# Kernel optimization log

Measured on AMD Instinct MI355X. Metric: run time of the kernel, lower is better.

## Reference

```python
import jax, jax.numpy as jnp
import numpy as np

NUM_SAMPLES = 1024  # from init_kwargs


def _fps(x, num_samples):
    """Iterative farthest-point sampling.

    x: [B, N, C] float point cloud.
    Returns (sampled_points [B, S, C], indices [B, S] int32).
    Starts from point 0 in each cloud (deterministic seed point).
    """
    B, N, C = x.shape
    barange = jnp.arange(B)
    init_idx = jnp.zeros((B,), dtype=jnp.int32)
    init_min = jnp.full((B, N), jnp.inf, dtype=x.dtype)

    def step(carry, _):
        min_d, cur = carry
        pt = x[barange, cur]                                  # [B, C] current farthest point
        d = jnp.sum((x - pt[:, None, :]) ** 2, axis=-1)       # [B, N] squared dist to it
        min_d = jnp.minimum(min_d, d)                         # running min-dist to sampled set
        nxt = jnp.argmax(min_d, axis=1).astype(jnp.int32)     # next farthest point per cloud
        return (min_d, nxt), cur                              # emit the index we just consumed

    (_, _), idxs = jax.lax.scan(step, (init_min, init_idx), None, length=num_samples)
    idxs = jnp.transpose(idxs)                                # [B, S]
    sampled = jnp.take_along_axis(x, idxs[..., None], axis=1)  # [B, S, C]
    return sampled, idxs


def setup_inputs() -> dict:
    key = jax.random.key(0)
    x = jax.random.uniform(key, (64, 32768, 3), dtype=jnp.float32)
    return {"x": x}


def reference(x):
    return _fps(x, NUM_SAMPLES)
```

## Files before the change

kernel.cpp:

```cpp
#include <hip/hip_runtime.h>


typedef unsigned long long u64;
typedef unsigned int u32;
typedef unsigned short u16;

#define FPS_N   32768
#define FPS_S   1024
#define FPS_NT  1024
#define NCELL   512
#define PPT     (FPS_N / FPS_NT)

__device__ __forceinline__ int bin_of(float v) {
    int i = (int)(v * 8.0f);
    i = i < 0 ? 0 : (i > 7 ? 7 : i);
    if (v < (float)i * 0.125f) --i;
    if (v >= (float)(i + 1) * 0.125f) ++i;
    i = i < 0 ? 0 : (i > 7 ? 7 : i);
    return i;
}

__global__ __launch_bounds__(FPS_NT) void FPSModel_80753975099708_kernel(
    const float* __restrict__ x,
    float* __restrict__ out_pts,
    float* __restrict__ out_idx,
    float4* __restrict__ ws4)
{
#pragma clang fp contract(off)
    const int b = blockIdx.x;
    const int t = threadIdx.x;
    const int w = t >> 6;
    const int lane = t & 63;
    const float* __restrict__ xb = x + (size_t)b * FPS_N * 3;
    float* __restrict__ op = out_pts + (size_t)b * FPS_S * 3;
    float* __restrict__ oi = out_idx + (size_t)b * FPS_S;
    float4* __restrict__ srt = ws4 + (size_t)b * FPS_N;

    __shared__ float mind[FPS_N];
    __shared__ u32  cellCnt[NCELL];
    __shared__ u32  cellStart[NCELL + 1];
    __shared__ u64  bkey[NCELL];
    __shared__ float bwx[NCELL], bwy[NCELL], bwz[NCELL];
    __shared__ u16  wl[2][NCELL];
    __shared__ u32  nD[2];
    __shared__ u64  redk[16];
    __shared__ float redx[16], redy[16], redz[16];

    if (t < NCELL) cellCnt[t] = 0;
    if (t == 0) { nD[0] = 0; nD[1] = 0; }
    __syncthreads();

#pragma unroll
    for (int k = 0; k < PPT; ++k) {
        const int i = k * FPS_NT + t;
        mind[i] = __int_as_float(0x7f800000);
        const float gx = xb[3 * i], gy = xb[3 * i + 1], gz = xb[3 * i + 2];
        const int c = (bin_of(gx) << 6) | (bin_of(gy) << 3) | bin_of(gz);
        atomicAdd(&cellCnt[c], 1u);
    }
    __syncthreads();

    if (t == 0) {
        u32 acc = 0;
        for (int c = 0; c < NCELL; ++c) { cellStart[c] = acc; acc += cellCnt[c]; }
        cellStart[NCELL] = acc;
    }
    __syncthreads();
    if (t < NCELL) cellCnt[t] = cellStart[t];
    __syncthreads();

#pragma unroll
    for (int k = 0; k < PPT; ++k) {
        const int i = k * FPS_NT + t;
        const float gx = xb[3 * i], gy = xb[3 * i + 1], gz = xb[3 * i + 2];
        const int c = (bin_of(gx) << 6) | (bin_of(gy) << 3) | bin_of(gz);
        const u32 slot = atomicAdd(&cellCnt[c], 1u);
        float4 q;
        q.x = gx; q.y = gy; q.z = gz; q.w = __uint_as_float((u32)i);
        srt[slot] = q;
    }
    if (t < NCELL) {
        bkey[t] = (cellStart[t + 1] > cellStart[t])
                      ? 0x7f80000000000000ULL
                      : 0ULL;
        bwx[t] = 0.f; bwy[t] = 0.f; bwz[t] = 0.f;
    }

    float px = xb[0], py = xb[1], pz = xb[2];
    if (t == 0) {
        oi[0] = 0.0f;
        op[0] = px; op[1] = py; op[2] = pz;
    }
    __syncthreads();

    for (int s = 1; s < FPS_S; ++s) {
        const int p = s & 1;
        if (t == 0) nD[1 - p] = 0;
        if (t < NCELL) {
            const int ix = (t >> 6) & 7, iy = (t >> 3) & 7, iz = t & 7;
            const float lox = (float)ix * 0.125f;
            const float loy = (float)iy * 0.125f;
            const float loz = (float)iz * 0.125f;
            const float ax = fmaxf(fmaxf(lox - px, px - (lox + 0.125f)), 0.0f);
            const float ay = fmaxf(fmaxf(loy - py, py - (loy + 0.125f)), 0.0f);
            const float az = fmaxf(fmaxf(loz - pz, pz - (loz + 0.125f)), 0.0f);
            const float lb2 = ax * ax + ay * ay + az * az;
            const float bmax = __uint_as_float((u32)(bkey[t] >> 32));
            if (!(lb2 >= bmax * 1.000004f)) {
                wl[p][atomicAdd(&nD[p], 1u)] = (u16)t;
            }
        }
        __syncthreads();

        const int nd = (int)nD[p];
        for (int wi = w; wi < nd; wi += 16) {
            const int c = wl[p][wi];
            const int start = (int)cellStart[c], end = (int)cellStart[c + 1];
            u64 bk = 0; float bx = 0.f, by = 0.f, bz = 0.f;
            for (int off = start; off < end; off += 64) {
                const int l = off + lane;
                if (l < end) {
                    const float4 q = srt[l];
                    const float dx = q.x - px;
                    const float dy = q.y - py;
                    const float dz = q.z - pz;
                    const float d = __builtin_fmaf(dz, dz,
                                     __builtin_fmaf(dx, dx, dy * dy));
                    const float m = fminf(mind[l], d);
                    mind[l] = m;
                    const u64 key = ((u64)__float_as_uint(m) << 32) |
                                    (u64)(0xFFFFFFFFu - __float_as_uint(q.w));
                    if (key > bk) { bk = key; bx = q.x; by = q.y; bz = q.z; }
                }
            }
#pragma unroll
            for (int o = 32; o; o >>= 1) {
                const u64 ok = __shfl_xor((unsigned long long)bk, o);
                const float ox = __shfl_xor(bx, o);
                const float oy = __shfl_xor(by, o);
                const float oz = __shfl_xor(bz, o);
                if (ok > bk) { bk = ok; bx = ox; by = oy; bz = oz; }
            }
            if (lane == 0) { bkey[c] = bk; bwx[c] = bx; bwy[c] = by; bwz[c] = bz; }
        }
        __syncthreads();

        u64 k = 0; float wx = 0.f, wy = 0.f, wz = 0.f;
        if (t < NCELL) { k = bkey[t]; wx = bwx[t]; wy = bwy[t]; wz = bwz[t]; }
#pragma unroll
        for (int o = 32; o; o >>= 1) {
            const u64 ok = __shfl_xor((unsigned long long)k, o);
            const float ox = __shfl_xor(wx, o);
            const float oy = __shfl_xor(wy, o);
            const float oz = __shfl_xor(wz, o);
            if (ok > k) { k = ok; wx = ox; wy = oy; wz = oz; }
        }
        if (lane == 0) { redk[w] = k; redx[w] = wx; redy[w] = wy; redz[w] = wz; }
        __syncthreads();

        u64 fk = redk[0];
        float fx = redx[0], fy = redy[0], fz = redz[0];
#pragma unroll
        for (int j = 1; j < 16; ++j) {
            const u64 kk = redk[j];
            if (kk > fk) { fk = kk; fx = redx[j]; fy = redy[j]; fz = redz[j]; }
        }
        px = fx; py = fy; pz = fz;

        if (t == 0) {
            oi[s] = (float)(int)(0xFFFFFFFFu - (u32)(fk & 0xFFFFFFFFull));
            op[(size_t)s * 3 + 0] = fx;
            op[(size_t)s * 3 + 1] = fy;
            op[(size_t)s * 3 + 2] = fz;
        }
    }
}

extern "C" void kernel_launch(void* const* d_in, const int* in_sizes, int n_in,
                              void* d_out, int out_size, void* d_ws, size_t ws_size,
                              hipStream_t stream) {
    const float* x = (const float*)d_in[0];
    const int B = in_sizes[0] / (FPS_N * 3);

    float* out_pts = (float*)d_out;
    float* out_idx = out_pts + (size_t)B * FPS_S * 3;
    float4* ws4 = (float4*)d_ws;

    hipLaunchKernelGGL(FPSModel_80753975099708_kernel,
                       dim3(B), dim3(FPS_NT), 0, stream,
                       x, out_pts, out_idx, ws4);
}
```

Measured before the change: 4.493 ms.

## Coarsen grid to 64 cells, compute dirty set per wave via ballot, drop a barrier

Reduces the spatial grid from 512 to 64 cells so every wave can compute the dirty-cell bitmask itself with a ballot over its lanes. This removes the shared worklist, its atomics and one barrier per step. Cell bests are double-buffered, and the final argmax is a serial scan of 64 keys per thread. Coordinates of the new point are reloaded from global memory, and a software prefetch is added to the cell scan loop. The cost is that coarser cells prune less, so more points are rescanned each step, and the dirty cells are load-balanced round-robin across waves.

```diff
diff --git a/kernel.cpp b/kernel.cpp
--- a/kernel.cpp
+++ b/kernel.cpp
@@ -3,20 +3,19 @@
 
 typedef unsigned long long u64;
 typedef unsigned int u32;
-typedef unsigned short u16;
 
 #define FPS_N   32768
 #define FPS_S   1024
 #define FPS_NT  1024
-#define NCELL   512
+#define NCELL   64
 #define PPT     (FPS_N / FPS_NT)
 
-__device__ __forceinline__ int bin_of(float v) {
-    int i = (int)(v * 8.0f);
-    i = i < 0 ? 0 : (i > 7 ? 7 : i);
-    if (v < (float)i * 0.125f) --i;
-    if (v >= (float)(i + 1) * 0.125f) ++i;
-    i = i < 0 ? 0 : (i > 7 ? 7 : i);
+__device__ __forceinline__ int bin4(float v) {
+    int i = (int)(v * 4.0f);
+    i = i < 0 ? 0 : (i > 3 ? 3 : i);
+    if (v < (float)i * 0.25f) --i;
+    if (v >= (float)(i + 1) * 0.25f) ++i;
+    i = i < 0 ? 0 : (i > 3 ? 3 : i);
     return i;
 }
 
@@ -37,17 +36,11 @@
     float4* __restrict__ srt = ws4 + (size_t)b * FPS_N;
 
     __shared__ float mind[FPS_N];
-    __shared__ u32  cellCnt[NCELL];
+    __shared__ u64  bkey[2][NCELL];
     __shared__ u32  cellStart[NCELL + 1];
-    __shared__ u64  bkey[NCELL];
-    __shared__ float bwx[NCELL], bwy[NCELL], bwz[NCELL];
-    __shared__ u16  wl[2][NCELL];
-    __shared__ u32  nD[2];
-    __shared__ u64  redk[16];
-    __shared__ float redx[16], redy[16], redz[16];
+    __shared__ u32  cellCur[NCELL];
 
-    if (t < NCELL) cellCnt[t] = 0;
-    if (t == 0) { nD[0] = 0; nD[1] = 0; }
+    if (t < NCELL) cellCur[t] = 0;
     __syncthreads();
 
 #pragma unroll
@@ -55,35 +48,34 @@
         const int i = k * FPS_NT + t;
         mind[i] = __int_as_float(0x7f800000);
         const float gx = xb[3 * i], gy = xb[3 * i + 1], gz = xb[3 * i + 2];
-        const int c = (bin_of(gx) << 6) | (bin_of(gy) << 3) | bin_of(gz);
-        atomicAdd(&cellCnt[c], 1u);
+        const int c = (bin4(gx) << 4) | (bin4(gy) << 2) | bin4(gz);
+        atomicAdd(&cellCur[c], 1u);
     }
     __syncthreads();
 
     if (t == 0) {
         u32 acc = 0;
-        for (int c = 0; c < NCELL; ++c) { cellStart[c] = acc; acc += cellCnt[c]; }
+        for (int c = 0; c < NCELL; ++c) { cellStart[c] = acc; acc += cellCur[c]; }
         cellStart[NCELL] = acc;
     }
     __syncthreads();
-    if (t < NCELL) cellCnt[t] = cellStart[t];
+    if (t < NCELL) cellCur[t] = cellStart[t];
     __syncthreads();
 
 #pragma unroll
     for (int k = 0; k < PPT; ++k) {
         const int i = k * FPS_NT + t;
         const float gx = xb[3 * i], gy = xb[3 * i + 1], gz = xb[3 * i + 2];
-        const int c = (bin_of(gx) << 6) | (bin_of(gy) << 3) | bin_of(gz);
-        const u32 slot = atomicAdd(&cellCnt[c], 1u);
+        const int c = (bin4(gx) << 4) | (bin4(gy) << 2) | bin4(gz);
+        const u32 slot = atomicAdd(&cellCur[c], 1u);
         float4 q;
         q.x = gx; q.y = gy; q.z = gz; q.w = __uint_as_float((u32)i);
         srt[slot] = q;
     }
     if (t < NCELL) {
-        bkey[t] = (cellStart[t + 1] > cellStart[t])
-                      ? 0x7f80000000000000ULL
-                      : 0ULL;
-        bwx[t] = 0.f; bwy[t] = 0.f; bwz[t] = 0.f;
+        bkey[0][t] = (cellStart[t + 1] > cellStart[t])
+                         ? 0x7f80000000000000ULL
+                         : 0ULL;
     }
 
     float px = xb[0], py = xb[1], pz = xb[2];
@@ -94,84 +86,81 @@
     __syncthreads();
 
     for (int s = 1; s < FPS_S; ++s) {
-        const int p = s & 1;
-        if (t == 0) nD[1 - p] = 0;
-        if (t < NCELL) {
-            const int ix = (t >> 6) & 7, iy = (t >> 3) & 7, iz = t & 7;
-            const float lox = (float)ix * 0.125f;
-            const float loy = (float)iy * 0.125f;
-            const float loz = (float)iz * 0.125f;
-            const float ax = fmaxf(fmaxf(lox - px, px - (lox + 0.125f)), 0.0f);
-            const float ay = fmaxf(fmaxf(loy - py, py - (loy + 0.125f)), 0.0f);
-            const float az = fmaxf(fmaxf(loz - pz, pz - (loz + 0.125f)), 0.0f);
-            const float lb2 = ax * ax + ay * ay + az * az;
-            const float bmax = __uint_as_float((u32)(bkey[t] >> 32));
-            if (!(lb2 >= bmax * 1.000004f)) {
-                wl[p][atomicAdd(&nD[p], 1u)] = (u16)t;
+        const int p  = s & 1;
+        const int qb = p ^ 1;
+
+        const int ix = (lane >> 4) & 3, iy = (lane >> 2) & 3, iz = lane & 3;
+        const float lox = (float)ix * 0.25f;
+        const float loy = (float)iy * 0.25f;
+        const float loz = (float)iz * 0.25f;
+        const float ax = fmaxf(fmaxf(lox - px, px - (lox + 0.25f)), 0.0f);
+        const float ay = fmaxf(fmaxf(loy - py, py - (loy + 0.25f)), 0.0f);
+        const float az = fmaxf(fmaxf(loz - pz, pz - (loz + 0.25f)), 0.0f);
+        const float lb2 = ax * ax + ay * ay + az * az;
+        const u64 prevk = bkey[qb][lane];
+        const float bmax = __uint_as_float((u32)(prevk >> 32));
+        const bool dirty = !(lb2 >= bmax * 1.000004f);
+        const u64 mask = __ballot(dirty);
+
+        if (w == 0 && !dirty) bkey[p][lane] = prevk;
+
+        u64 mrem = mask;
+        int j = 0;
+        while (mrem) {
+            const int c = __ffsll((unsigned long long)mrem) - 1;
+            mrem &= mrem - 1;
+            if ((j & 15) == w) {
+                const int end = (int)cellStart[c + 1];
+                int off = (int)cellStart[c] + lane;
+                u64 bk = 0;
+                float4 q0;
+                if (off < end) q0 = srt[off];
+                while (off < end) {
+                    const int off2 = off + 64;
+                    float4 q1;
+                    if (off2 < end) q1 = srt[off2];
+                    const float dx = q0.x - px;
+                    const float dy = q0.y - py;
+                    const float dz = q0.z - pz;
+                    const float d = __builtin_fmaf(dz, dz,
+                                     __builtin_fmaf(dx, dx, dy * dy));
+                    const float m = fminf(mind[off], d);
+                    mind[off] = m;
+                    const u64 key = ((u64)__float_as_uint(m) << 32) |
+                                    (u64)(0xFFFFFFFFu - __float_as_uint(q0.w));
+                    if (key > bk) bk = key;
+                    q0 = q1;
+                    off = off2;
+                }
+#pragma unroll
+                for (int o = 32; o; o >>= 1) {
+                    const u64 ok = __shfl_xor((unsigned long long)bk, o);
+                    if (ok > bk) bk = ok;
+                }
+                if (lane == 0) bkey[p][c] = bk;
             }
+            ++j;
         }
         __syncthreads();
 
-        const int nd = (int)nD[p];
-        for (int wi = w; wi < nd; wi += 16) {
-            const int c = wl[p][wi];
-            const int start = (int)cellStart[c], end = (int)cellStart[c + 1];
-            u64 bk = 0; float bx = 0.f, by = 0.f, bz = 0.f;
-            for (int off = start; off < end; off += 64) {
-                const int l = off + lane;
-                if (l < end) {
-                    const float4 q = srt[l];
-                    const float dx = q.x - px;
-                    const float dy = q.y - py;
-                    const float dz = q.z - pz;
-                    const float d = __builtin_fmaf(dz, dz,
-                                     __builtin_fmaf(dx, dx, dy * dy));
-                    const float m = fminf(mind[l], d);
-                    mind[l] = m;
-                    const u64 key = ((u64)__float_as_uint(m) << 32) |
-                                    (u64)(0xFFFFFFFFu - __float_as_uint(q.w));
-                    if (key > bk) { bk = key; bx = q.x; by = q.y; bz = q.z; }
-                }
-            }
+        u64 fk = bkey[p][0];
 #pragma unroll
-            for (int o = 32; o; o >>= 1) {
-                const u64 ok = __shfl_xor((unsigned long long)bk, o);
-                const float ox = __shfl_xor(bx, o);
-                const float oy = __shfl_xor(by, o);
-                const float oz = __shfl_xor(bz, o);
-                if (ok > bk) { bk = ok; bx = ox; by = oy; bz = oz; }
-            }
-            if (lane == 0) { bkey[c] = bk; bwx[c] = bx; bwy[c] = by; bwz[c] = bz; }
+        for (int jj = 1; jj < NCELL; ++jj) {
+            const u64 kk = bkey[p][jj];
+            if (kk > fk) fk = kk;
         }
-        __syncthreads();
+        const int cur = (int)(0xFFFFFFFFu - (u32)(fk & 0xFFFFFFFFull));
 
-        u64 k = 0; float wx = 0.f, wy = 0.f, wz = 0.f;
-        if (t < NCELL) { k = bkey[t]; wx = bwx[t]; wy = bwy[t]; wz = bwz[t]; }
-#pragma unroll
-        for (int o = 32; o; o >>= 1) {
-            const u64 ok = __shfl_xor((unsigned long long)k, o);
-            const float ox = __shfl_xor(wx, o);
-            const float oy = __shfl_xor(wy, o);
-            const float oz = __shfl_xor(wz, o);
-            if (ok > k) { k = ok; wx = ox; wy = oy; wz = oz; }
-        }
-        if (lane == 0) { redk[w] = k; redx[w] = wx; redy[w] = wy; redz[w] = wz; }
-        __syncthreads();
-
-        u64 fk = redk[0];
-        float fx = redx[0], fy = redy[0], fz = redz[0];
-#pragma unroll
-        for (int j = 1; j < 16; ++j) {
-            const u64 kk = redk[j];
-            if (kk > fk) { fk = kk; fx = redx[j]; fy = redy[j]; fz = redz[j]; }
-        }
-        px = fx; py = fy; pz = fz;
+        const int curU = __builtin_amdgcn_readfirstlane(cur);
+        px = xb[3 * curU + 0];
+        py = xb[3 * curU + 1];
+        pz = xb[3 * curU + 2];
 
         if (t == 0) {
-            oi[s] = (float)(int)(0xFFFFFFFFu - (u32)(fk & 0xFFFFFFFFull));
-            op[(size_t)s * 3 + 0] = fx;
-            op[(size_t)s * 3 + 1] = fy;
-            op[(size_t)s * 3 + 2] = fz;
+            oi[s] = (float)cur;
+            op[(size_t)s * 3 + 0] = px;
+            op[(size_t)s * 3 + 1] = py;
+            op[(size_t)s * 3 + 2] = pz;
         }
     }
 }
```

Result: faster. 3.800 ms (-15.4%).

## Use fixed 64-point spatially sorted chunks with AABB pruning and ballot worklists

Applied to the files above, without the earlier changes.

Points are still counting-sorted into 512 grid cells, but pruning now works on 512 fixed chunks of 64 consecutive sorted points, each with its own bounding box computed by wave reductions. The dirty-chunk list is built from ballots instead of a shared atomic worklist. Chunk work is split round-robin across waves, with the next chunk loaded before the previous one is processed. The per-chunk winner reduction shuffles only the key and resolves coordinates through a chunk index, cutting shuffle traffic. The tighter boxes should prune more tightly than the fixed grid cells, but chunks can straddle cells and so have looser bounds.

```diff
diff --git a/kernel.cpp b/kernel.cpp
--- a/kernel.cpp
+++ b/kernel.cpp
@@ -3,15 +3,15 @@
 
 typedef unsigned long long u64;
 typedef unsigned int u32;
-typedef unsigned short u16;
 
 #define FPS_N   32768
 #define FPS_S   1024
 #define FPS_NT  1024
-#define NCELL   512
+#define NCH     512
+#define NCELL9  512
 #define PPT     (FPS_N / FPS_NT)
 
-__device__ __forceinline__ int bin_of(float v) {
+__device__ __forceinline__ int bin8(float v) {
     int i = (int)(v * 8.0f);
     i = i < 0 ? 0 : (i > 7 ? 7 : i);
     if (v < (float)i * 0.125f) --i;
@@ -37,17 +37,17 @@
     float4* __restrict__ srt = ws4 + (size_t)b * FPS_N;
 
     __shared__ float mind[FPS_N];
-    __shared__ u32  cellCnt[NCELL];
-    __shared__ u32  cellStart[NCELL + 1];
-    __shared__ u64  bkey[NCELL];
-    __shared__ float bwx[NCELL], bwy[NCELL], bwz[NCELL];
-    __shared__ u16  wl[2][NCELL];
-    __shared__ u32  nD[2];
-    __shared__ u64  redk[16];
-    __shared__ float redx[16], redy[16], redz[16];
-
-    if (t < NCELL) cellCnt[t] = 0;
-    if (t == 0) { nD[0] = 0; nD[1] = 0; }
+    __shared__ float alox[NCH], aloy[NCH], aloz[NCH];
+    __shared__ float ahix[NCH], ahiy[NCH], ahiz[NCH];
+    __shared__ u64  ckey[NCH];
+    __shared__ float cwx[NCH], cwy[NCH], cwz[NCH];
+    __shared__ u64  dmask[8];
+    __shared__ u64  wkey[8];
+    __shared__ u32  wchunk[8];
+    __shared__ u32  cellStart[NCELL9 + 1];
+    __shared__ u32  cellCur[NCELL9];
+
+    if (t < NCELL9) cellCur[t] = 0;
     __syncthreads();
 
 #pragma unroll
@@ -55,35 +55,48 @@
         const int i = k * FPS_NT + t;
         mind[i] = __int_as_float(0x7f800000);
         const float gx = xb[3 * i], gy = xb[3 * i + 1], gz = xb[3 * i + 2];
-        const int c = (bin_of(gx) << 6) | (bin_of(gy) << 3) | bin_of(gz);
-        atomicAdd(&cellCnt[c], 1u);
-    }
-    __syncthreads();
-
+        const int c = (bin8(gx) << 6) | (bin8(gy) << 3) | bin8(gz);
+        atomicAdd(&cellCur[c], 1u);
+    }
+    __syncthreads();
     if (t == 0) {
         u32 acc = 0;
-        for (int c = 0; c < NCELL; ++c) { cellStart[c] = acc; acc += cellCnt[c]; }
-        cellStart[NCELL] = acc;
-    }
-    __syncthreads();
-    if (t < NCELL) cellCnt[t] = cellStart[t];
-    __syncthreads();
-
+        for (int c = 0; c < NCELL9; ++c) { cellStart[c] = acc; acc += cellCur[c]; }
+        cellStart[NCELL9] = acc;
+    }
+    __syncthreads();
+    if (t < NCELL9) cellCur[t] = cellStart[t];
+    __syncthreads();
 #pragma unroll
     for (int k = 0; k < PPT; ++k) {
         const int i = k * FPS_NT + t;
         const float gx = xb[3 * i], gy = xb[3 * i + 1], gz = xb[3 * i + 2];
-        const int c = (bin_of(gx) << 6) | (bin_of(gy) << 3) | bin_of(gz);
-        const u32 slot = atomicAdd(&cellCnt[c], 1u);
+        const int c = (bin8(gx) << 6) | (bin8(gy) << 3) | bin8(gz);
+        const u32 slot = atomicAdd(&cellCur[c], 1u);
         float4 q;
         q.x = gx; q.y = gy; q.z = gz; q.w = __uint_as_float((u32)i);
         srt[slot] = q;
     }
-    if (t < NCELL) {
-        bkey[t] = (cellStart[t + 1] > cellStart[t])
-                      ? 0x7f80000000000000ULL
-                      : 0ULL;
-        bwx[t] = 0.f; bwy[t] = 0.f; bwz[t] = 0.f;
+    __syncthreads();
+
+    for (int c = w; c < NCH; c += 16) {
+        const float4 q = srt[(c << 6) + lane];
+        float mnx = q.x, mny = q.y, mnz = q.z;
+        float mxx = q.x, mxy = q.y, mxz = q.z;
+#pragma unroll
+        for (int o = 32; o; o >>= 1) {
+            mnx = fminf(mnx, __shfl_xor(mnx, o));
+            mny = fminf(mny, __shfl_xor(mny, o));
+            mnz = fminf(mnz, __shfl_xor(mnz, o));
+            mxx = fmaxf(mxx, __shfl_xor(mxx, o));
+            mxy = fmaxf(mxy, __shfl_xor(mxy, o));
+            mxz = fmaxf(mxz, __shfl_xor(mxz, o));
+        }
+        if (lane == 0) {
+            alox[c] = mnx; aloy[c] = mny; aloz[c] = mnz;
+            ahix[c] = mxx; ahiy[c] = mxy; ahiz[c] = mxz;
+            ckey[c] = 0x7f80000000000000ULL;
+        }
     }
 
     float px = xb[0], py = xb[1], pz = xb[2];
@@ -94,84 +107,90 @@
     __syncthreads();
 
     for (int s = 1; s < FPS_S; ++s) {
-        const int p = s & 1;
-        if (t == 0) nD[1 - p] = 0;
-        if (t < NCELL) {
-            const int ix = (t >> 6) & 7, iy = (t >> 3) & 7, iz = t & 7;
-            const float lox = (float)ix * 0.125f;
-            const float loy = (float)iy * 0.125f;
-            const float loz = (float)iz * 0.125f;
-            const float ax = fmaxf(fmaxf(lox - px, px - (lox + 0.125f)), 0.0f);
-            const float ay = fmaxf(fmaxf(loy - py, py - (loy + 0.125f)), 0.0f);
-            const float az = fmaxf(fmaxf(loz - pz, pz - (loz + 0.125f)), 0.0f);
+        if (w < 8) {
+            const int c = (w << 6) | lane;
+            const float bmax = __uint_as_float((u32)(ckey[c] >> 32));
+            const float ax = fmaxf(fmaxf(alox[c] - px, px - ahix[c]), 0.0f);
+            const float ay = fmaxf(fmaxf(aloy[c] - py, py - ahiy[c]), 0.0f);
+            const float az = fmaxf(fmaxf(aloz[c] - pz, pz - ahiz[c]), 0.0f);
             const float lb2 = ax * ax + ay * ay + az * az;
-            const float bmax = __uint_as_float((u32)(bkey[t] >> 32));
-            if (!(lb2 >= bmax * 1.000004f)) {
-                wl[p][atomicAdd(&nD[p], 1u)] = (u16)t;
-            }
+            const bool dirty = !(lb2 >= bmax * 1.000004f);
+            const u64 mk = __ballot(dirty);
+            if (lane == 0) dmask[w] = mk;
         }
         __syncthreads();
 
-        const int nd = (int)nD[p];
-        for (int wi = w; wi < nd; wi += 16) {
-            const int c = wl[p][wi];
-            const int start = (int)cellStart[c], end = (int)cellStart[c + 1];
-            u64 bk = 0; float bx = 0.f, by = 0.f, bz = 0.f;
-            for (int off = start; off < end; off += 64) {
-                const int l = off + lane;
-                if (l < end) {
-                    const float4 q = srt[l];
-                    const float dx = q.x - px;
-                    const float dy = q.y - py;
-                    const float dz = q.z - pz;
-                    const float d = __builtin_fmaf(dz, dz,
-                                     __builtin_fmaf(dx, dx, dy * dy));
-                    const float m = fminf(mind[l], d);
-                    mind[l] = m;
-                    const u64 key = ((u64)__float_as_uint(m) << 32) |
-                                    (u64)(0xFFFFFFFFu - __float_as_uint(q.w));
-                    if (key > bk) { bk = key; bx = q.x; by = q.y; bz = q.z; }
-                }
-            }
+        auto PROCESS = [&](int c, float4 q) {
+            const int slot = (c << 6) + lane;
+            const float dx = q.x - px;
+            const float dy = q.y - py;
+            const float dz = q.z - pz;
+            const float d = __builtin_fmaf(dz, dz,
+                             __builtin_fmaf(dx, dx, dy * dy));
+            const float m = fminf(mind[slot], d);
+            mind[slot] = m;
+            const u64 key = ((u64)__float_as_uint(m) << 32) |
+                            (u64)(0xFFFFFFFFu - __float_as_uint(q.w));
+            u64 bk = key;
 #pragma unroll
             for (int o = 32; o; o >>= 1) {
                 const u64 ok = __shfl_xor((unsigned long long)bk, o);
-                const float ox = __shfl_xor(bx, o);
-                const float oy = __shfl_xor(by, o);
-                const float oz = __shfl_xor(bz, o);
-                if (ok > bk) { bk = ok; bx = ox; by = oy; bz = oz; }
-            }
-            if (lane == 0) { bkey[c] = bk; bwx[c] = bx; bwy[c] = by; bwz[c] = bz; }
-        }
+                if (ok > bk) bk = ok;
+            }
+            if (key == bk) {
+                ckey[c] = bk;
+                cwx[c] = q.x; cwy[c] = q.y; cwz[c] = q.z;
+            }
+        };
+
+        int J = 0, cPrev = -1;
+        float4 qPrev;
+        for (int w8 = 0; w8 < 8; ++w8) {
+            u64 m = dmask[w8];
+            while (m) {
+                const int bit = __ffsll((unsigned long long)m) - 1;
+                m &= m - 1;
+                if ((J & 15) == w) {
+                    const int c = (w8 << 6) | bit;
+                    const float4 qNew = srt[(c << 6) + lane];
+                    if (cPrev >= 0) PROCESS(cPrev, qPrev);
+                    qPrev = qNew; cPrev = c;
+                }
+                ++J;
+            }
+        }
+        if (cPrev >= 0) PROCESS(cPrev, qPrev);
         __syncthreads();
 
-        u64 k = 0; float wx = 0.f, wy = 0.f, wz = 0.f;
-        if (t < NCELL) { k = bkey[t]; wx = bwx[t]; wy = bwy[t]; wz = bwz[t]; }
-#pragma unroll
-        for (int o = 32; o; o >>= 1) {
-            const u64 ok = __shfl_xor((unsigned long long)k, o);
-            const float ox = __shfl_xor(wx, o);
-            const float oy = __shfl_xor(wy, o);
-            const float oz = __shfl_xor(wz, o);
-            if (ok > k) { k = ok; wx = ox; wy = oy; wz = oz; }
-        }
-        if (lane == 0) { redk[w] = k; redx[w] = wx; redy[w] = wy; redz[w] = wz; }
+        if (w < 8) {
+            const int c0 = (w << 6) | lane;
+            u64 kk = ckey[c0];
+            u32 cc = (u32)c0;
+#pragma unroll
+            for (int o = 32; o; o >>= 1) {
+                const u64 ok = __shfl_xor((unsigned long long)kk, o);
+                const u32 oc = (u32)__shfl_xor((int)cc, o);
+                if (ok > kk) { kk = ok; cc = oc; }
+            }
+            if (lane == 0) { wkey[w] = kk; wchunk[w] = cc; }
+        }
         __syncthreads();
 
-        u64 fk = redk[0];
-        float fx = redx[0], fy = redy[0], fz = redz[0];
-#pragma unroll
-        for (int j = 1; j < 16; ++j) {
-            const u64 kk = redk[j];
-            if (kk > fk) { fk = kk; fx = redx[j]; fy = redy[j]; fz = redz[j]; }
-        }
-        px = fx; py = fy; pz = fz;
+        u64 fk = wkey[0];
+        u32 fc = wchunk[0];
+#pragma unroll
+        for (int j = 1; j < 8; ++j) {
+            const u64 kk = wkey[j];
+            if (kk > fk) { fk = kk; fc = wchunk[j]; }
+        }
+        const int cur = (int)(0xFFFFFFFFu - (u32)(fk & 0xFFFFFFFFull));
+        px = cwx[fc]; py = cwy[fc]; pz = cwz[fc];
 
         if (t == 0) {
-            oi[s] = (float)(int)(0xFFFFFFFFu - (u32)(fk & 0xFFFFFFFFull));
-            op[(size_t)s * 3 + 0] = fx;
-            op[(size_t)s * 3 + 1] = fy;
-            op[(size_t)s * 3 + 2] = fz;
+            oi[s] = (float)cur;
+            op[(size_t)s * 3 + 0] = px;
+            op[(size_t)s * 3 + 1] = py;
+            op[(size_t)s * 3 + 2] = pz;
         }
     }
 }
```

New measurement: 4.570 ms. Within noise of the previous version (+1.7%).
